# Optimization experiments

Hardware: AMD Instinct MI355X
Metric: run time of the kernel (lower is better)

## Reference

```python
import jax, jax.numpy as jnp
import numpy as np

S, O, A, R = 32, 64, 8, 8   # s_nvals, o_nvals, a_nvals, r_nvals
B, T = 1024, 128            # batch of episodes, n_transitions


def setup_inputs() -> dict:
    key = jax.random.key(0)
    ks = jax.random.split(key, 10)
    regime = jax.random.randint(ks[0], (B,), 0, 2).astype(jnp.float32)
    obs = jax.random.randint(ks[1], (T + 1, B), 0, O)
    rewards = jax.random.randint(ks[2], (T + 1, B), 0, R)
    dones = (jax.random.uniform(ks[3], (T + 1, B)) < 0.02).astype(jnp.float32)
    actions = jax.random.randint(ks[4], (T, B), 0, A)
    params_s = jax.random.normal(ks[5], (S,), dtype=jnp.float32)
    params_s_sa = jax.random.normal(ks[6], (S, A, S), dtype=jnp.float32)
    params_o_s = jax.random.normal(ks[7], (S, O), dtype=jnp.float32)
    params_r_s = jax.random.normal(ks[8], (S, R), dtype=jnp.float32)
    params_a_s = jax.random.normal(ks[9], (S, A), dtype=jnp.float32)
    return {
        "regime": regime, "obs": obs, "rewards": rewards, "dones": dones,
        "actions": actions, "params_s": params_s, "params_s_sa": params_s_sa,
        "params_o_s": params_o_s, "params_r_s": params_r_s, "params_a_s": params_a_s,
    }


def _log_prob(regime, obs, rewards, dones, actions,
              params_s, params_s_sa, params_o_s, params_r_s, params_a_s):
    """Batched HMM forward-filtering log p(o_{0:T}, r_{0:T}, a_{0:T-1}) (with_done=False)."""
    log_pi = jax.nn.log_softmax(params_s, axis=-1)      # [S]
    log_Tr = jax.nn.log_softmax(params_s_sa, axis=-1)   # [S, A, S']
    log_Os = jax.nn.log_softmax(params_o_s, axis=-1)    # [S, O]
    log_Rs = jax.nn.log_softmax(params_r_s, axis=-1)    # [S, R]
    log_As = jax.nn.log_softmax(params_a_s, axis=-1)    # [S, A]
    log_Tr_a = jnp.transpose(log_Tr, (1, 0, 2))          # [A, S, S']
    Bsz = regime.shape[0]
    regime_mask = (regime == 1.0)[:, None]               # [B, 1]

    def step(carry, xs):
        log_q_s_hprev, log_prob, was_done = carry        # [B,S], [B], [B]
        o, r, d, a = xs                                  # each [B]
        done = jnp.maximum(was_done, d)
        log_q_o = log_Os.T[o]                            # [B, S]
        log_q_r = log_Rs.T[r]                            # [B, S]
        log_q_a = log_As.T[a]                            # [B, S]
        log_q_a = jnp.where((done == 1.0)[:, None] | regime_mask, 0.0, log_q_a)
        log_q_sorda = log_q_s_hprev + log_q_o + log_q_r + log_q_a   # [B, S]
        log_q_orda = jax.nn.logsumexp(log_q_sorda, axis=-1) * (1.0 - was_done)
        log_prob = jnp.where(jnp.isinf(log_prob), log_prob, log_prob + log_q_orda)
        log_q_s_h = log_q_sorda - log_q_orda[:, None]    # posterior over s_t, [B, S]
        # predict: logsumexp over s of q(s|h) * p(s'|s,a)  -> [B, S']
        log_q_snext = jax.nn.logsumexp(log_q_s_h[:, :, None] + log_Tr_a[a], axis=1)
        return (log_q_snext, log_prob, done), None

    init = (jnp.broadcast_to(log_pi, (Bsz, S)),
            jnp.zeros((Bsz,), log_pi.dtype),
            jnp.zeros((Bsz,), dones.dtype))
    (log_q_s_hprev, log_prob, was_done), _ = jax.lax.scan(
        step, init, (obs[:-1], rewards[:-1], dones[:-1], actions))

    # final step t = T: no action term, no transition
    log_q_sord = log_q_s_hprev + log_Os.T[obs[-1]] + log_Rs.T[rewards[-1]]
    log_q_ord = jax.nn.logsumexp(log_q_sord, axis=-1) * (1.0 - was_done)
    log_prob = jnp.where(jnp.isinf(log_prob), log_prob, log_prob + log_q_ord)
    return log_prob


def reference(regime, obs, rewards, dones, actions,
              params_s, params_s_sa, params_o_s, params_r_s, params_a_s):
    return _log_prob(regime, obs, rewards, dones, actions,
                     params_s, params_s_sa, params_o_s, params_r_s, params_a_s)
```

## Files before the change

### kernel.cpp

```cpp
#include <hip/hip_runtime.h>

#define S_N 32
#define O_N 64
#define A_N 8
#define R_N 8
#define B_N 1024
#define T_N 128

#define OT_OFF   4096
#define RA_OFF   6144
#define RT_OFF   8192
#define PI_OFF   8448

#define L_OT 0
#define L_RA 2048
#define L_RT 4096
#define L_PI 4352
#define L_N  4384

typedef float f32x4 __attribute__((ext_vector_type(4)));
typedef short bf16x8 __attribute__((ext_vector_type(8)));

__global__ __launch_bounds__(256) void tam_prep(
    const float* __restrict__ params_s,
    const float* __restrict__ params_s_sa,
    const float* __restrict__ params_o_s,
    const float* __restrict__ params_r_s,
    const float* __restrict__ params_a_s,
    float* __restrict__ ws)
{
    const int tid = threadIdx.x;
    if (blockIdx.x == 0) {
        const int s = tid >> 3, a = tid & 7;
        const float* row = params_s_sa + (s * A_N + a) * S_N;
        float p[32];
        #pragma unroll
        for (int i = 0; i < 8; ++i) {
            float4 v = reinterpret_cast<const float4*>(row)[i];
            p[4*i]=v.x; p[4*i+1]=v.y; p[4*i+2]=v.z; p[4*i+3]=v.w;
        }
        float mx = p[0];
        #pragma unroll
        for (int i = 1; i < 32; ++i) mx = fmaxf(mx, p[i]);
        float sum = 0.f;
        #pragma unroll
        for (int i = 0; i < 32; ++i) { p[i] = __expf(p[i] - mx); sum += p[i]; }
        const float inv = 1.0f / sum;
        unsigned short* wsh = reinterpret_cast<unsigned short*>(ws);
        #pragma unroll
        for (int d = 0; d < 32; ++d) {
            const unsigned bits = __float_as_uint(p[d] * inv) + 0x8000u;
            const int idx = ((a * 2 + (d >> 4)) * 64 + 16 * (s >> 3) + (d & 15)) * 8
                            + (s & 7);
            wsh[idx] = (unsigned short)(bits >> 16);
        }
    } else {
        __shared__ float sRT[256], sAT[256];
        if (tid < 32) {
            const int s = tid;
            const float* row = params_o_s + s * O_N;
            float p[64];
            #pragma unroll
            for (int i = 0; i < 16; ++i) {
                float4 v = reinterpret_cast<const float4*>(row)[i];
                p[4*i]=v.x; p[4*i+1]=v.y; p[4*i+2]=v.z; p[4*i+3]=v.w;
            }
            float mx = p[0];
            #pragma unroll
            for (int i = 1; i < 64; ++i) mx = fmaxf(mx, p[i]);
            float sum = 0.f;
            #pragma unroll
            for (int i = 0; i < 64; ++i) { p[i] = __expf(p[i] - mx); sum += p[i]; }
            const float inv = 1.0f / sum;
            #pragma unroll
            for (int o = 0; o < 64; ++o) ws[OT_OFF + o * 32 + s] = p[o] * inv;
        } else if (tid < 64) {
            const int s = tid - 32;
            const float* row = params_r_s + s * R_N;
            float p[8];
            #pragma unroll
            for (int i = 0; i < 2; ++i) {
                float4 v = reinterpret_cast<const float4*>(row)[i];
                p[4*i]=v.x; p[4*i+1]=v.y; p[4*i+2]=v.z; p[4*i+3]=v.w;
            }
            float mx = p[0];
            #pragma unroll
            for (int i = 1; i < 8; ++i) mx = fmaxf(mx, p[i]);
            float sum = 0.f;
            #pragma unroll
            for (int i = 0; i < 8; ++i) { p[i] = __expf(p[i] - mx); sum += p[i]; }
            const float inv = 1.0f / sum;
            #pragma unroll
            for (int r = 0; r < 8; ++r) {
                const float v = p[r] * inv;
                ws[RT_OFF + r * 32 + s] = v;
                sRT[r * 32 + s] = v;
            }
        } else if (tid < 96) {
            const int s = tid - 64;
            const float* row = params_a_s + s * A_N;
            float p[8];
            #pragma unroll
            for (int i = 0; i < 2; ++i) {
                float4 v = reinterpret_cast<const float4*>(row)[i];
                p[4*i]=v.x; p[4*i+1]=v.y; p[4*i+2]=v.z; p[4*i+3]=v.w;
            }
            float mx = p[0];
            #pragma unroll
            for (int i = 1; i < 8; ++i) mx = fmaxf(mx, p[i]);
            float sum = 0.f;
            #pragma unroll
            for (int i = 0; i < 8; ++i) { p[i] = __expf(p[i] - mx); sum += p[i]; }
            const float inv = 1.0f / sum;
            #pragma unroll
            for (int a = 0; a < 8; ++a) sAT[a * 32 + s] = p[a] * inv;
        } else if (tid < 128) {
            const int s = tid - 96;
            float p[32];
            #pragma unroll
            for (int i = 0; i < 8; ++i) {
                float4 v = reinterpret_cast<const float4*>(params_s)[i];
                p[4*i]=v.x; p[4*i+1]=v.y; p[4*i+2]=v.z; p[4*i+3]=v.w;
            }
            float mx = p[0];
            #pragma unroll
            for (int i = 1; i < 32; ++i) mx = fmaxf(mx, p[i]);
            float sum = 0.f;
            #pragma unroll
            for (int i = 0; i < 32; ++i) { p[i] = __expf(p[i] - mx); sum += p[i]; }
            ws[PI_OFF + s] = p[s] / sum;
        }
        __syncthreads();
        #pragma unroll 1
        for (int i = tid; i < 2048; i += 256) {
            const int sl = i & 31, ra = i >> 5;
            ws[RA_OFF + i] = sRT[(ra >> 3) * 32 + sl] * sAT[(ra & 7) * 32 + sl];
        }
    }
}

#define RLI(v, l) __builtin_amdgcn_readlane((v), (l))

#define LOADT(TH0, TH1, A_) {                                                \
    const bf16x8* p_ = reinterpret_cast<const bf16x8*>(sTH + ((A_) << 7));   \
    TH0 = p_[lane];                                                          \
    TH1 = p_[lane + 64]; }

#define LOADE(E, PKW) {                                                      \
    const unsigned pk_ = (PKW);                                              \
    const float eo_  = sE[(int)(pk_ & 63u) * 32 + sl];                       \
    const float era_ = sE[eBase + (int)((pk_ >> 6) & 7u) * eMulR             \
                        + (int)((pk_ >> 9) & 7u) * eMulA + sl];              \
    E = eo_ * era_; }

#define STEP(E, TH0, TH1) {                                                  \
    const float wv = u * (E);                                                \
    const int wvb = __float_as_int(wv) + 0x8000;                             \
    const int wpb = __builtin_amdgcn_mov_dpp(wvb, 0xB1, 0xF, 0xF, true);     \
    const int whi = (int)(((unsigned)wvb >> 16) |                            \
                          ((unsigned)wpb & 0xffff0000u));                    \
    union { int i[4]; bf16x8 v; } A_;                                        \
    A_.i[0] = __builtin_amdgcn_ds_bpermute(bpb,      whi);                   \
    A_.i[1] = __builtin_amdgcn_ds_bpermute(bpb + 8,  whi);                   \
    A_.i[2] = __builtin_amdgcn_ds_bpermute(bpb + 16, whi);                   \
    A_.i[3] = __builtin_amdgcn_ds_bpermute(bpb + 24, whi);                   \
    const f32x4 d0 = __builtin_amdgcn_mfma_f32_16x16x32_bf16(A_.v, TH0, zf4, 0, 0, 0); \
    const f32x4 d1 = __builtin_amdgcn_mfma_f32_16x16x32_bf16(A_.v, TH1, zf4, 0, 0, 0); \
    u = (lane & 16) ? d1[0] : d0[0];                                         \
}

#define RESCALE() {                                                          \
    const int ub = RLI(__float_as_int(u), 0);                                \
    const int kb = (ub >> 23) & 255;                                         \
    u *= __int_as_float((254 - kb) << 23);                                   \
    ksum += kb - 127; }

__global__ __launch_bounds__(256) void tam_main(
    const float* __restrict__ regime,
    const int*   __restrict__ obs,
    const int*   __restrict__ rewards,
    const int*   __restrict__ dones_i,
    const int*   __restrict__ actions,
    const float* __restrict__ ws,
    float* __restrict__ out)
{
    __shared__ uint4 sTH[1024];
    __shared__ float sE[L_N];
    const int tid  = threadIdx.x;
    const int lane = tid & 63;
    const int wid  = tid >> 6;
    const int sl   = lane & 31;
    const int bpb  = (lane >> 4) * 32;
    const int b    = blockIdx.x * 4 + wid;
    const f32x4 zf4 = {0.f, 0.f, 0.f, 0.f};

    {
        const uint4* gt = reinterpret_cast<const uint4*>(ws);
        #pragma unroll
        for (int i = 0; i < 4; ++i) sTH[tid + i * 256] = gt[tid + i * 256];
        const float4* ge = reinterpret_cast<const float4*>(ws + OT_OFF);
        float4* s4 = reinterpret_cast<float4*>(sE);
        #pragma unroll 1
        for (int i = tid; i < L_N / 4; i += 256) s4[i] = ge[i];
    }
    __syncthreads();

    const int t0 = 2 * lane, t1 = 2 * lane + 1;
    const int o0 = obs[t0 * B_N + b],      o1 = obs[t1 * B_N + b];
    const int r0 = rewards[t0 * B_N + b],  r1 = rewards[t1 * B_N + b];
    const int a0 = actions[t0 * B_N + b],  a1 = actions[t1 * B_N + b];
    const int d0i = dones_i[t0 * B_N + b], d1i = dones_i[t1 * B_N + b];
    const int vpk = (o0 | (r0 << 6) | (a0 << 9)) |
                    ((o1 | (r1 << 6) | (a1 << 9)) << 16);

    const unsigned long long mEv = __ballot(d0i != 0);
    const unsigned long long mOd = __ballot(d1i != 0);
    const int tE = mEv ? 2 * __builtin_ctzll(mEv)     : (1 << 30);
    const int tO = mOd ? 2 * __builtin_ctzll(mOd) + 1 : (1 << 30);
    const int tstar  = tE < tO ? tE : tO;
    const int nsteps = tstar < 128 ? tstar : 128;

    const bool skipA = (regime[b] == 1.0f);
    const int eBase = skipA ? L_RT : L_RA;
    const int eMulR = skipA ? 32 : 256;
    const int eMulA = skipA ? 0 : 32;

    float u = sE[L_PI + sl];
    int ksum = 0;
    float eA, eB;
    bf16x8 thA0, thA1, thB0, thB1;

    unsigned pkc = (unsigned)RLI(vpk, 0);
    unsigned pkn = (unsigned)RLI(vpk, 1);
    LOADE(eA, pkc & 0xffffu);
    LOADT(thA0, thA1, (int)((pkc >> 9) & 7u));

    const int npairs = nsteps >> 1;
    #pragma unroll 1
    for (int i = 0; i < npairs; ++i) {
        LOADE(eB, pkc >> 16);
        LOADT(thB0, thB1, (int)((pkc >> 25) & 7u));
        STEP(eA, thA0, thA1);
        LOADE(eA, pkn & 0xffffu);
        LOADT(thA0, thA1, (int)((pkn >> 9) & 7u));
        STEP(eB, thB0, thB1);
        pkc = pkn;
        pkn = (unsigned)RLI(vpk, i + 2);
        RESCALE();
    }

    if (nsteps & 1) {
        STEP(eA, thA0, thA1);
    }

    {
        const int e  = nsteps;
        const int oe = obs[e * B_N + b];
        const int re = rewards[e * B_N + b];
        const float eo = sE[L_OT + oe * 32 + sl];
        const float rt = sE[L_RT + re * 32 + sl];
        float t = u * eo * rt;
        t += __shfl_xor(t, 1, 32);
        t += __shfl_xor(t, 2, 32);
        t += __shfl_xor(t, 4, 32);
        t += __shfl_xor(t, 8, 32);
        t += __shfl_xor(t, 16, 32);
        const float result = (float)ksum * 0.69314718055994531f + __logf(t);
        if (lane == 0) out[b] = result;
    }
}

extern "C" void kernel_launch(void* const* d_in, const int* in_sizes, int n_in,
                              void* d_out, int out_size, void* d_ws, size_t ws_size,
                              hipStream_t stream) {
    (void)in_sizes; (void)n_in; (void)out_size; (void)ws_size;
    const float* regime      = (const float*)d_in[0];
    const int*   obs         = (const int*)d_in[1];
    const int*   rewards     = (const int*)d_in[2];
    const int*   dones_i     = (const int*)d_in[3];
    const int*   actions     = (const int*)d_in[4];
    const float* params_s    = (const float*)d_in[5];
    const float* params_s_sa = (const float*)d_in[6];
    const float* params_o_s  = (const float*)d_in[7];
    const float* params_r_s  = (const float*)d_in[8];
    const float* params_a_s  = (const float*)d_in[9];
    float* ws  = (float*)d_ws;
    float* out = (float*)d_out;

    tam_prep<<<2, 256, 0, stream>>>(params_s, params_s_sa, params_o_s,
                                    params_r_s, params_a_s, ws);
    tam_main<<<256, 256, 0, stream>>>(regime, obs, rewards, dones_i, actions, ws, out);
}
```

Before: 29.11 us.

## Fuse parameter softmax prep into main kernel and split state across half-lanes

Removes the separate prep kernel and global workspace round trip: every block now recomputes the log-softmax tables (transition bf16 tiles, emission, reward/action products, prior) directly into shared memory before running the forward filter. The state vector layout also changes so each lane holds two states (lo/hi halves), which removes the DPP swap and lane-select after the MFMA, and the final reduction drops to 16 lanes. The intent is to cut one kernel launch and its serialization; in exchange every block redoes the parameter softmax work (256 rows of 32 for transitions), which adds startup latency per block.

```diff
diff --git a/kernel.cpp b/kernel.cpp
--- a/kernel.cpp
+++ b/kernel.cpp
@@ -7,11 +7,6 @@
 #define B_N 1024
 #define T_N 128
 
-#define OT_OFF   4096
-#define RA_OFF   6144
-#define RT_OFF   8192
-#define PI_OFF   8448
-
 #define L_OT 0
 #define L_RA 2048
 #define L_RT 4096
@@ -21,187 +16,176 @@
 typedef float f32x4 __attribute__((ext_vector_type(4)));
 typedef short bf16x8 __attribute__((ext_vector_type(8)));
 
-__global__ __launch_bounds__(256) void tam_prep(
+#define RLI(v, l) __builtin_amdgcn_readlane((v), (l))
+
+#define LOADT(TH0, TH1, A_) {                                                \
+    const bf16x8* p_ = reinterpret_cast<const bf16x8*>(sTH + ((A_) << 7));   \
+    TH0 = p_[lane];                                                          \
+    TH1 = p_[lane + 64]; }
+
+#define LOADE(ELO, EHI, PKW) {                                               \
+    const unsigned pk_ = (PKW);                                              \
+    const int ob_ = L_OT + (int)(pk_ & 63u) * 32 + h0;                       \
+    const int rb_ = eBase + (int)((pk_ >> 6) & 7u) * eMulR                   \
+                  + (int)((pk_ >> 9) & 7u) * eMulA + h0;                     \
+    ELO = sE[ob_] * sE[rb_];                                                 \
+    EHI = sE[ob_ + 16] * sE[rb_ + 16]; }
+
+#define STEP(ELO, EHI, TH0, TH1) {                                           \
+    const float wlo = ulo * (ELO), whi = uhi * (EHI);                        \
+    const int ilo = __float_as_int(wlo) + 0x8000;                            \
+    const int ihi = __float_as_int(whi) + 0x8000;                            \
+    const int pw = (int)(((unsigned)ilo >> 16) | ((unsigned)ihi & 0xffff0000u)); \
+    union { int i[4]; bf16x8 v; } A_;                                        \
+    A_.i[0] = __builtin_amdgcn_ds_bpermute(bpb,      pw);                    \
+    A_.i[1] = __builtin_amdgcn_ds_bpermute(bpb + 4,  pw);                    \
+    A_.i[2] = __builtin_amdgcn_ds_bpermute(bpb + 8,  pw);                    \
+    A_.i[3] = __builtin_amdgcn_ds_bpermute(bpb + 12, pw);                    \
+    const f32x4 d0 = __builtin_amdgcn_mfma_f32_16x16x32_bf16(A_.v, TH0, zf4, 0, 0, 0); \
+    const f32x4 d1 = __builtin_amdgcn_mfma_f32_16x16x32_bf16(A_.v, TH1, zf4, 0, 0, 0); \
+    ulo = d0[0]; uhi = d1[0];                                                \
+}
+
+#define RESCALE() {                                                          \
+    const int ub = RLI(__float_as_int(ulo), 0);                              \
+    const int kb = (ub >> 23) & 255;                                         \
+    const float sc_ = __int_as_float((254 - kb) << 23);                      \
+    ulo *= sc_; uhi *= sc_;                                                  \
+    ksum += kb - 127; }
+
+__global__ __launch_bounds__(256) void tam_fused(
+    const float* __restrict__ regime,
+    const int*   __restrict__ obs,
+    const int*   __restrict__ rewards,
+    const int*   __restrict__ dones_i,
+    const int*   __restrict__ actions,
     const float* __restrict__ params_s,
     const float* __restrict__ params_s_sa,
     const float* __restrict__ params_o_s,
     const float* __restrict__ params_r_s,
     const float* __restrict__ params_a_s,
-    float* __restrict__ ws)
-{
-    const int tid = threadIdx.x;
-    if (blockIdx.x == 0) {
-        const int s = tid >> 3, a = tid & 7;
-        const float* row = params_s_sa + (s * A_N + a) * S_N;
-        float p[32];
-        #pragma unroll
-        for (int i = 0; i < 8; ++i) {
-            float4 v = reinterpret_cast<const float4*>(row)[i];
-            p[4*i]=v.x; p[4*i+1]=v.y; p[4*i+2]=v.z; p[4*i+3]=v.w;
-        }
-        float mx = p[0];
-        #pragma unroll
-        for (int i = 1; i < 32; ++i) mx = fmaxf(mx, p[i]);
-        float sum = 0.f;
-        #pragma unroll
-        for (int i = 0; i < 32; ++i) { p[i] = __expf(p[i] - mx); sum += p[i]; }
-        const float inv = 1.0f / sum;
-        unsigned short* wsh = reinterpret_cast<unsigned short*>(ws);
-        #pragma unroll
-        for (int d = 0; d < 32; ++d) {
-            const unsigned bits = __float_as_uint(p[d] * inv) + 0x8000u;
-            const int idx = ((a * 2 + (d >> 4)) * 64 + 16 * (s >> 3) + (d & 15)) * 8
-                            + (s & 7);
-            wsh[idx] = (unsigned short)(bits >> 16);
-        }
-    } else {
-        __shared__ float sRT[256], sAT[256];
-        if (tid < 32) {
-            const int s = tid;
-            const float* row = params_o_s + s * O_N;
-            float p[64];
-            #pragma unroll
-            for (int i = 0; i < 16; ++i) {
-                float4 v = reinterpret_cast<const float4*>(row)[i];
-                p[4*i]=v.x; p[4*i+1]=v.y; p[4*i+2]=v.z; p[4*i+3]=v.w;
-            }
-            float mx = p[0];
-            #pragma unroll
-            for (int i = 1; i < 64; ++i) mx = fmaxf(mx, p[i]);
-            float sum = 0.f;
-            #pragma unroll
-            for (int i = 0; i < 64; ++i) { p[i] = __expf(p[i] - mx); sum += p[i]; }
-            const float inv = 1.0f / sum;
-            #pragma unroll
-            for (int o = 0; o < 64; ++o) ws[OT_OFF + o * 32 + s] = p[o] * inv;
-        } else if (tid < 64) {
-            const int s = tid - 32;
-            const float* row = params_r_s + s * R_N;
-            float p[8];
-            #pragma unroll
-            for (int i = 0; i < 2; ++i) {
-                float4 v = reinterpret_cast<const float4*>(row)[i];
-                p[4*i]=v.x; p[4*i+1]=v.y; p[4*i+2]=v.z; p[4*i+3]=v.w;
-            }
-            float mx = p[0];
-            #pragma unroll
-            for (int i = 1; i < 8; ++i) mx = fmaxf(mx, p[i]);
-            float sum = 0.f;
-            #pragma unroll
-            for (int i = 0; i < 8; ++i) { p[i] = __expf(p[i] - mx); sum += p[i]; }
-            const float inv = 1.0f / sum;
-            #pragma unroll
-            for (int r = 0; r < 8; ++r) {
-                const float v = p[r] * inv;
-                ws[RT_OFF + r * 32 + s] = v;
-                sRT[r * 32 + s] = v;
-            }
-        } else if (tid < 96) {
-            const int s = tid - 64;
-            const float* row = params_a_s + s * A_N;
-            float p[8];
-            #pragma unroll
-            for (int i = 0; i < 2; ++i) {
-                float4 v = reinterpret_cast<const float4*>(row)[i];
-                p[4*i]=v.x; p[4*i+1]=v.y; p[4*i+2]=v.z; p[4*i+3]=v.w;
-            }
-            float mx = p[0];
-            #pragma unroll
-            for (int i = 1; i < 8; ++i) mx = fmaxf(mx, p[i]);
-            float sum = 0.f;
-            #pragma unroll
-            for (int i = 0; i < 8; ++i) { p[i] = __expf(p[i] - mx); sum += p[i]; }
-            const float inv = 1.0f / sum;
-            #pragma unroll
-            for (int a = 0; a < 8; ++a) sAT[a * 32 + s] = p[a] * inv;
-        } else if (tid < 128) {
-            const int s = tid - 96;
-            float p[32];
-            #pragma unroll
-            for (int i = 0; i < 8; ++i) {
-                float4 v = reinterpret_cast<const float4*>(params_s)[i];
-                p[4*i]=v.x; p[4*i+1]=v.y; p[4*i+2]=v.z; p[4*i+3]=v.w;
-            }
-            float mx = p[0];
-            #pragma unroll
-            for (int i = 1; i < 32; ++i) mx = fmaxf(mx, p[i]);
-            float sum = 0.f;
-            #pragma unroll
-            for (int i = 0; i < 32; ++i) { p[i] = __expf(p[i] - mx); sum += p[i]; }
-            ws[PI_OFF + s] = p[s] / sum;
-        }
-        __syncthreads();
-        #pragma unroll 1
-        for (int i = tid; i < 2048; i += 256) {
-            const int sl = i & 31, ra = i >> 5;
-            ws[RA_OFF + i] = sRT[(ra >> 3) * 32 + sl] * sAT[(ra & 7) * 32 + sl];
-        }
-    }
-}
-
-#define RLI(v, l) __builtin_amdgcn_readlane((v), (l))
-
-#define LOADT(TH0, TH1, A_) {                                                \
-    const bf16x8* p_ = reinterpret_cast<const bf16x8*>(sTH + ((A_) << 7));   \
-    TH0 = p_[lane];                                                          \
-    TH1 = p_[lane + 64]; }
-
-#define LOADE(E, PKW) {                                                      \
-    const unsigned pk_ = (PKW);                                              \
-    const float eo_  = sE[(int)(pk_ & 63u) * 32 + sl];                       \
-    const float era_ = sE[eBase + (int)((pk_ >> 6) & 7u) * eMulR             \
-                        + (int)((pk_ >> 9) & 7u) * eMulA + sl];              \
-    E = eo_ * era_; }
-
-#define STEP(E, TH0, TH1) {                                                  \
-    const float wv = u * (E);                                                \
-    const int wvb = __float_as_int(wv) + 0x8000;                             \
-    const int wpb = __builtin_amdgcn_mov_dpp(wvb, 0xB1, 0xF, 0xF, true);     \
-    const int whi = (int)(((unsigned)wvb >> 16) |                            \
-                          ((unsigned)wpb & 0xffff0000u));                    \
-    union { int i[4]; bf16x8 v; } A_;                                        \
-    A_.i[0] = __builtin_amdgcn_ds_bpermute(bpb,      whi);                   \
-    A_.i[1] = __builtin_amdgcn_ds_bpermute(bpb + 8,  whi);                   \
-    A_.i[2] = __builtin_amdgcn_ds_bpermute(bpb + 16, whi);                   \
-    A_.i[3] = __builtin_amdgcn_ds_bpermute(bpb + 24, whi);                   \
-    const f32x4 d0 = __builtin_amdgcn_mfma_f32_16x16x32_bf16(A_.v, TH0, zf4, 0, 0, 0); \
-    const f32x4 d1 = __builtin_amdgcn_mfma_f32_16x16x32_bf16(A_.v, TH1, zf4, 0, 0, 0); \
-    u = (lane & 16) ? d1[0] : d0[0];                                         \
-}
-
-#define RESCALE() {                                                          \
-    const int ub = RLI(__float_as_int(u), 0);                                \
-    const int kb = (ub >> 23) & 255;                                         \
-    u *= __int_as_float((254 - kb) << 23);                                   \
-    ksum += kb - 127; }
-
-__global__ __launch_bounds__(256) void tam_main(
-    const float* __restrict__ regime,
-    const int*   __restrict__ obs,
-    const int*   __restrict__ rewards,
-    const int*   __restrict__ dones_i,
-    const int*   __restrict__ actions,
-    const float* __restrict__ ws,
     float* __restrict__ out)
 {
     __shared__ uint4 sTH[1024];
     __shared__ float sE[L_N];
+    __shared__ float sAT[256];
     const int tid  = threadIdx.x;
     const int lane = tid & 63;
     const int wid  = tid >> 6;
-    const int sl   = lane & 31;
-    const int bpb  = (lane >> 4) * 32;
+    const int h0   = lane & 15;
+    const int g    = lane >> 4;
+    const int bpb  = g * 16;
     const int b    = blockIdx.x * 4 + wid;
     const f32x4 zf4 = {0.f, 0.f, 0.f, 0.f};
 
-    {
-        const uint4* gt = reinterpret_cast<const uint4*>(ws);
-        #pragma unroll
-        for (int i = 0; i < 4; ++i) sTH[tid + i * 256] = gt[tid + i * 256];
-        const float4* ge = reinterpret_cast<const float4*>(ws + OT_OFF);
-        float4* s4 = reinterpret_cast<float4*>(sE);
+    if (tid < 128) {
+        unsigned short* sTHh = reinterpret_cast<unsigned short*>(sTH);
         #pragma unroll 1
-        for (int i = tid; i < L_N / 4; i += 256) s4[i] = ge[i];
+        for (int rr = 0; rr < 2; ++rr) {
+            const int idx = 2 * tid + rr;
+            const int s = idx >> 3, a = idx & 7;
+            const float* row = params_s_sa + (s * A_N + a) * S_N;
+            float p[32];
+            #pragma unroll
+            for (int i = 0; i < 8; ++i) {
+                float4 v = reinterpret_cast<const float4*>(row)[i];
+                p[4*i]=v.x; p[4*i+1]=v.y; p[4*i+2]=v.z; p[4*i+3]=v.w;
+            }
+            float mx = p[0];
+            #pragma unroll
+            for (int i = 1; i < 32; ++i) mx = fmaxf(mx, p[i]);
+            float sum = 0.f;
+            #pragma unroll
+            for (int i = 0; i < 32; ++i) { p[i] = __expf(p[i] - mx); sum += p[i]; }
+            const float inv = 1.0f / sum;
+            const int ks = 2 * (s & 15) + (s >> 4);
+            const int gk = ks >> 3, e8 = ks & 7;
+            #pragma unroll
+            for (int d = 0; d < 32; ++d) {
+                const unsigned bits = __float_as_uint(p[d] * inv) + 0x8000u;
+                const int l2 = 16 * gk + (d & 15);
+                sTHh[((a * 2 + (d >> 4)) * 64 + l2) * 8 + e8] =
+                    (unsigned short)(bits >> 16);
+            }
+        }
+    } else {
+        const int e = tid - 128;
+        if (e < 32) {
+            const int s = e;
+            const float* row = params_o_s + s * O_N;
+            float p[64];
+            #pragma unroll
+            for (int i = 0; i < 16; ++i) {
+                float4 v = reinterpret_cast<const float4*>(row)[i];
+                p[4*i]=v.x; p[4*i+1]=v.y; p[4*i+2]=v.z; p[4*i+3]=v.w;
+            }
+            float mx = p[0];
+            #pragma unroll
+            for (int i = 1; i < 64; ++i) mx = fmaxf(mx, p[i]);
+            float sum = 0.f;
+            #pragma unroll
+            for (int i = 0; i < 64; ++i) { p[i] = __expf(p[i] - mx); sum += p[i]; }
+            const float inv = 1.0f / sum;
+            #pragma unroll
+            for (int o = 0; o < 64; ++o) sE[L_OT + o * 32 + s] = p[o] * inv;
+        } else if (e < 64) {
+            const int s = e - 32;
+            const float* row = params_r_s + s * R_N;
+            float p[8];
+            #pragma unroll
+            for (int i = 0; i < 2; ++i) {
+                float4 v = reinterpret_cast<const float4*>(row)[i];
+                p[4*i]=v.x; p[4*i+1]=v.y; p[4*i+2]=v.z; p[4*i+3]=v.w;
+            }
+            float mx = p[0];
+            #pragma unroll
+            for (int i = 1; i < 8; ++i) mx = fmaxf(mx, p[i]);
+            float sum = 0.f;
+            #pragma unroll
+            for (int i = 0; i < 8; ++i) { p[i] = __expf(p[i] - mx); sum += p[i]; }
+            const float inv = 1.0f / sum;
+            #pragma unroll
+            for (int r = 0; r < 8; ++r) sE[L_RT + r * 32 + s] = p[r] * inv;
+        } else if (e < 96) {
+            const int s = e - 64;
+            const float* row = params_a_s + s * A_N;
+            float p[8];
+            #pragma unroll
+            for (int i = 0; i < 2; ++i) {
+                float4 v = reinterpret_cast<const float4*>(row)[i];
+                p[4*i]=v.x; p[4*i+1]=v.y; p[4*i+2]=v.z; p[4*i+3]=v.w;
+            }
+            float mx = p[0];
+            #pragma unroll
+            for (int i = 1; i < 8; ++i) mx = fmaxf(mx, p[i]);
+            float sum = 0.f;
+            #pragma unroll
+            for (int i = 0; i < 8; ++i) { p[i] = __expf(p[i] - mx); sum += p[i]; }
+            const float inv = 1.0f / sum;
+            #pragma unroll
+            for (int a = 0; a < 8; ++a) sAT[a * 32 + s] = p[a] * inv;
+        } else {
+            const int s = e - 96;
+            float p[32];
+            #pragma unroll
+            for (int i = 0; i < 8; ++i) {
+                float4 v = reinterpret_cast<const float4*>(params_s)[i];
+                p[4*i]=v.x; p[4*i+1]=v.y; p[4*i+2]=v.z; p[4*i+3]=v.w;
+            }
+            float mx = p[0];
+            #pragma unroll
+            for (int i = 1; i < 32; ++i) mx = fmaxf(mx, p[i]);
+            float sum = 0.f;
+            #pragma unroll
+            for (int i = 0; i < 32; ++i) { p[i] = __expf(p[i] - mx); sum += p[i]; }
+            sE[L_PI + s] = p[s] / sum;
+        }
+    }
+    __syncthreads();
+    #pragma unroll 1
+    for (int i = tid; i < 2048; i += 256) {
+        const int sl2 = i & 31, ra = i >> 5;
+        sE[L_RA + i] = sE[L_RT + (ra >> 3) * 32 + sl2] * sAT[(ra & 7) * 32 + sl2];
     }
     __syncthreads();
 
@@ -225,46 +209,46 @@
     const int eMulR = skipA ? 32 : 256;
     const int eMulA = skipA ? 0 : 32;
 
-    float u = sE[L_PI + sl];
+    float ulo = sE[L_PI + h0];
+    float uhi = sE[L_PI + h0 + 16];
     int ksum = 0;
-    float eA, eB;
+    float eloA, ehiA, eloB, ehiB;
     bf16x8 thA0, thA1, thB0, thB1;
 
     unsigned pkc = (unsigned)RLI(vpk, 0);
     unsigned pkn = (unsigned)RLI(vpk, 1);
-    LOADE(eA, pkc & 0xffffu);
+    LOADE(eloA, ehiA, pkc & 0xffffu);
     LOADT(thA0, thA1, (int)((pkc >> 9) & 7u));
 
     const int npairs = nsteps >> 1;
     #pragma unroll 1
     for (int i = 0; i < npairs; ++i) {
-        LOADE(eB, pkc >> 16);
+        LOADE(eloB, ehiB, pkc >> 16);
         LOADT(thB0, thB1, (int)((pkc >> 25) & 7u));
-        STEP(eA, thA0, thA1);
-        LOADE(eA, pkn & 0xffffu);
+        STEP(eloA, ehiA, thA0, thA1);
+        LOADE(eloA, ehiA, pkn & 0xffffu);
         LOADT(thA0, thA1, (int)((pkn >> 9) & 7u));
-        STEP(eB, thB0, thB1);
+        STEP(eloB, ehiB, thB0, thB1);
         pkc = pkn;
         pkn = (unsigned)RLI(vpk, i + 2);
         RESCALE();
     }
 
     if (nsteps & 1) {
-        STEP(eA, thA0, thA1);
+        STEP(eloA, ehiA, thA0, thA1);
     }
 
     {
         const int e  = nsteps;
         const int oe = obs[e * B_N + b];
         const int re = rewards[e * B_N + b];
-        const float eo = sE[L_OT + oe * 32 + sl];
-        const float rt = sE[L_RT + re * 32 + sl];
-        float t = u * eo * rt;
-        t += __shfl_xor(t, 1, 32);
-        t += __shfl_xor(t, 2, 32);
-        t += __shfl_xor(t, 4, 32);
-        t += __shfl_xor(t, 8, 32);
-        t += __shfl_xor(t, 16, 32);
+        const int ob = L_OT + oe * 32 + h0;
+        const int rb = L_RT + re * 32 + h0;
+        float t = ulo * sE[ob] * sE[rb] + uhi * sE[ob + 16] * sE[rb + 16];
+        t += __shfl_xor(t, 1, 16);
+        t += __shfl_xor(t, 2, 16);
+        t += __shfl_xor(t, 4, 16);
+        t += __shfl_xor(t, 8, 16);
         const float result = (float)ksum * 0.69314718055994531f + __logf(t);
         if (lane == 0) out[b] = result;
     }
@@ -273,7 +257,7 @@
 extern "C" void kernel_launch(void* const* d_in, const int* in_sizes, int n_in,
                               void* d_out, int out_size, void* d_ws, size_t ws_size,
                               hipStream_t stream) {
-    (void)in_sizes; (void)n_in; (void)out_size; (void)ws_size;
+    (void)in_sizes; (void)n_in; (void)out_size; (void)d_ws; (void)ws_size;
     const float* regime      = (const float*)d_in[0];
     const int*   obs         = (const int*)d_in[1];
     const int*   rewards     = (const int*)d_in[2];
@@ -284,10 +268,9 @@
     const float* params_o_s  = (const float*)d_in[7];
     const float* params_r_s  = (const float*)d_in[8];
     const float* params_a_s  = (const float*)d_in[9];
-    float* ws  = (float*)d_ws;
     float* out = (float*)d_out;
 
-    tam_prep<<<2, 256, 0, stream>>>(params_s, params_s_sa, params_o_s,
-                                    params_r_s, params_a_s, ws);
-    tam_main<<<256, 256, 0, stream>>>(regime, obs, rewards, dones_i, actions, ws, out);
+    tam_fused<<<256, 256, 0, stream>>>(regime, obs, rewards, dones_i, actions,
+                                       params_s, params_s_sa, params_o_s,
+                                       params_r_s, params_a_s, out);
 }
```

Result: faster. 26.33 us (-9.5%).
